# Optimization experiments

Hardware: AMD Instinct MI355X
Metric: run time of the kernel (lower is better)

The kernel has to match this reference:

```python
import jax, jax.numpy as jnp
import numpy as np

GRID_SIZE = 16          # number of spline intervals; G+1 = 17 control points
KH, KW = 3, 3           # kernel size
EPS = 1e-8


def _extract_patches(x, kh, kw):
    """x: (B,H,W,C) -> patches (B,Ho,Wo,C,kh,kw), valid padding, stride 1."""
    B, H, W, C = x.shape
    Ho, Wo = H - kh + 1, W - kw + 1
    rows = []
    for i in range(kh):
        cols = []
        for j in range(kw):
            cols.append(x[:, i:i + Ho, j:j + Wo, :])  # (B,Ho,Wo,C)
        rows.append(jnp.stack(cols, axis=-1))          # (B,Ho,Wo,C,kw)
    return jnp.stack(rows, axis=-2)                    # (B,Ho,Wo,C,kh,kw)


def setup_inputs() -> dict:
    key = jax.random.key(0)
    k1, k2, k3, k4 = jax.random.split(key, 4)
    B, H, W, C, F = 4, 66, 66, 32, 64
    x = jax.random.normal(k1, (B, H, W, C), dtype=jnp.float32)
    control_points = jax.random.normal(k2, (F, C, KH, KW, GRID_SIZE + 1), dtype=jnp.float32) * 0.1
    w_spline = jax.random.normal(k3, (F, C, KH, KW), dtype=jnp.float32) * 0.1
    w_silu = jax.random.normal(k4, (F, C, KH, KW), dtype=jnp.float32) * 0.1
    bias = jnp.zeros((F,), dtype=jnp.float32)
    return {"x": x, "control_points": control_points, "w_spline": w_spline,
            "w_silu": w_silu, "bias": bias}


def reference(x, control_points, w_spline, w_silu, bias):
    # Fixed B-spline grid in [-1, 1]
    grid = jnp.linspace(-1.0, 1.0, GRID_SIZE + 1, dtype=x.dtype)  # (G+1,)
    grid_spacing = 2.0 / GRID_SIZE

    # Patch extraction (valid padding, stride 1)
    patches = _extract_patches(x, KH, KW)  # (B,Ho,Wo,C,kh,kw)

    # Linear B-spline (hat) basis with normalization
    xc = jnp.clip(patches, -1.0, 1.0)
    dist = jnp.abs(xc[..., None] - grid)                     # (B,Ho,Wo,C,kh,kw,G+1)
    w = jnp.maximum(0.0, 1.0 - dist / grid_spacing)
    basis = w / (jnp.sum(w, axis=-1, keepdims=True) + EPS)

    # K(x) = w_spline * spline(x) + w_silu * SiLU(x); reduce over (C,kh,kw) per filter
    cp_eff = w_spline[..., None] * control_points            # (F,C,kh,kw,G+1)
    spline_term = jnp.einsum('bhwcijg,fcijg->bhwf', basis, cp_eff)
    silu_term = jnp.einsum('bhwcij,fcij->bhwf', jax.nn.silu(patches), w_silu)

    return spline_term + silu_term + bias  # (B,Ho,Wo,F)
```

## Files before the change

### kernel.cpp

```cpp
#include <hip/hip_runtime.h>
#include <stdint.h>

typedef _Float16 half8 __attribute__((ext_vector_type(8)));
typedef float f32x16 __attribute__((ext_vector_type(16)));
typedef float f32x4  __attribute__((ext_vector_type(4)));

#define NTH2 340992
#define PREP_BLOCKS (NTH2 / 256)

__global__ __launch_bounds__(256) void kan_prep(
    const float* __restrict__ cp, const float* __restrict__ wspl,
    const float* __restrict__ wsil, _Float16* __restrict__ th2)
{
    int e  = blockIdx.x * 256 + threadIdx.x;
    int p  = e / 18944;
    int r  = e - p * 18944;
    int f  = r / 296;
    int cb = r - f * 296;
    int i  = p / 6;
    int jh = p - i * 6;
    int j  = jh >> 1;
    int h2 = jh & 1;
    float v = 0.0f;
    if (cb < 288) {
        int kk = h2 * 288 + cb;
        int c  = kk / 18;
        int m  = kk - c * 18;
        int base = ((f * 32 + c) * 3 + i) * 3 + j;
        v = (m < 17) ? wspl[base] * cp[base * 17 + m] : wsil[base];
    }
    th2[e] = (_Float16)v;
}

__global__ __launch_bounds__(128) void kan_main(
    const float* __restrict__ x, const _Float16* __restrict__ th2,
    const float* __restrict__ bias, float* __restrict__ out)
{
    __shared__ __align__(16) _Float16 lA[32 * 296];
    __shared__ __align__(16) _Float16 lB[64 * 296];

    const int bx  = blockIdx.x;
    const int ph  = bx >> 8;
    const int row = bx & 255;
    const int b   = row >> 6;
    const int ho  = row & 63;

    const int tid  = threadIdx.x;
    const int wf   = tid >> 6;
    const int lane = tid & 63;
    const int r31  = lane & 31;
    const int kh   = lane >> 5;

    const int ar = tid >> 2;
    const int cq = tid & 3;

    const char* thB = (const char*)th2;
    char* lBc = (char*)lB;
    char* lAc = (char*)lA;

    f32x16 acc;
    {
        float bv = bias[wf * 32 + r31];
#pragma unroll
        for (int r = 0; r < 16; ++r) acc[r] = bv;
    }

    const _Float16* pa = lA + r31 * 296 + kh * 8;
    const _Float16* pb = lB + (wf * 32 + r31) * 296 + kh * 8;

    for (int p = 0; p < 18; ++p) {
        const int i  = p / 6;
        const int jh = p - i * 6;
        const int j  = jh >> 1;
        const int h2 = jh & 1;

        {
            const char* gs = thB + (size_t)p * 37888 + wf * 1024 + lane * 16;
            char* ld = lBc + wf * 1024;
#pragma unroll
            for (int t = 0; t < 18; ++t)
                __builtin_amdgcn_global_load_lds(
                    (const __attribute__((address_space(1))) void*)(gs + t * 2048),
                    (__attribute__((address_space(3))) void*)(ld + t * 2048),
                    16, 0, 0);
            if (wf == 0)
                __builtin_amdgcn_global_load_lds(
                    (const __attribute__((address_space(1))) void*)(gs + 36864),
                    (__attribute__((address_space(3))) void*)(lBc + 36864),
                    16, 0, 0);
        }

        {
            const f32x4 xv = *(const f32x4*)(
                x + ((size_t)((b * 66 + ho + i) * 66 + ph * 32 + ar + j)) * 32
                  + h2 * 16 + cq * 4);
#pragma unroll
            for (int pr = 0; pr < 2; ++pr) {
                union { _Float16 h[36]; uint64_t q[9]; } pk;
#pragma unroll
                for (int d = 0; d < 2; ++d) {
                    float pv = xv[pr * 2 + d];
                    float u  = fmaf(fminf(1.0f, fmaxf(-1.0f, pv)), 8.0f, 8.0f);
#pragma unroll
                    for (int m = 0; m < 17; ++m)
                        pk.h[d * 18 + m] =
                            (_Float16)fmaxf(0.0f, 1.0f - fabsf(u - (float)m));
                    pk.h[d * 18 + 17] = (_Float16)(
                        pv * __builtin_amdgcn_rcpf(1.0f + __expf(-pv)));
                }
                uint64_t* dst = (uint64_t*)(lAc + ar * 592 + cq * 144 + pr * 72);
#pragma unroll
                for (int r = 0; r < 9; ++r) dst[r] = pk.q[r];
            }
        }

        __syncthreads();

#pragma unroll
        for (int s = 0; s < 18; ++s) {
            half8 a  = *(const half8*)(pa + s * 16);
            half8 bf = *(const half8*)(pb + s * 16);
            acc = __builtin_amdgcn_mfma_f32_32x32x16_f16(a, bf, acc, 0, 0, 0);
        }

        __syncthreads();
    }

    float* obase = out
        + ((size_t)((b * 64 + ho) * 64 + ph * 32)) * 64 + wf * 32;
#pragma unroll
    for (int r = 0; r < 16; ++r) {
        int rowD = (r & 3) + 8 * (r >> 2) + 4 * kh;
        obase[(size_t)rowD * 64 + r31] = acc[r];
    }
}

extern "C" void kernel_launch(void* const* d_in, const int* in_sizes, int n_in,
                              void* d_out, int out_size, void* d_ws, size_t ws_size,
                              hipStream_t stream) {
    const float* x    = (const float*)d_in[0];
    const float* cp   = (const float*)d_in[1];
    const float* wspl = (const float*)d_in[2];
    const float* wsil = (const float*)d_in[3];
    const float* bias = (const float*)d_in[4];
    float* out = (float*)d_out;

    _Float16* th2 = (_Float16*)d_ws;

    kan_prep<<<PREP_BLOCKS, 256, 0, stream>>>(cp, wspl, wsil, th2);
    kan_main<<<512, 128, 0, stream>>>(x, th2, bias, out);
}
```

Baseline: 100.5 us.

## Double-buffer weight tiles and split K across waves with smaller stages

The reduction is split into 36 smaller stages instead of 18, and weight tiles are double-buffered in LDS so the next stage's async global-to-LDS load runs while the current stage's MFMAs execute. Each wave now covers all 64 filters but only half of the K slices, and the two partial sums are combined through LDS at the end. The weight layout is reorganised into a padding-free interleaved form to match. The design relies on hand-written waitcnt counts, which is a correctness risk, and it adds more barriers plus a final reduction step.

```diff
diff --git a/kernel.cpp b/kernel.cpp
--- a/kernel.cpp
+++ b/kernel.cpp
@@ -3,32 +3,27 @@
 
 typedef _Float16 half8 __attribute__((ext_vector_type(8)));
 typedef float f32x16 __attribute__((ext_vector_type(16)));
-typedef float f32x4  __attribute__((ext_vector_type(4)));
 
-#define NTH2 340992
-#define PREP_BLOCKS (NTH2 / 256)
+#define NBH (36 * 9216)
+#define PREP_BLOCKS (NBH / 256)
 
 __global__ __launch_bounds__(256) void kan_prep(
     const float* __restrict__ cp, const float* __restrict__ wspl,
     const float* __restrict__ wsil, _Float16* __restrict__ th2)
 {
-    int e  = blockIdx.x * 256 + threadIdx.x;
-    int p  = e / 18944;
-    int r  = e - p * 18944;
-    int f  = r / 296;
-    int cb = r - f * 296;
-    int i  = p / 6;
-    int jh = p - i * 6;
-    int j  = jh >> 1;
-    int h2 = jh & 1;
-    float v = 0.0f;
-    if (cb < 288) {
-        int kk = h2 * 288 + cb;
-        int c  = kk / 18;
-        int m  = kk - c * 18;
-        int base = ((f * 32 + c) * 3 + i) * 3 + j;
-        v = (m < 17) ? wspl[base] * cp[base * 17 + m] : wsil[base];
-    }
+    int e = blockIdx.x * 256 + threadIdx.x;
+    int p = e / 9216;
+    int r = e - p * 9216;
+    int u = r >> 3, h = r & 7;
+    int off = u >> 6, f = u & 63;
+    int i = p / 12;
+    int rr = p - i * 12;
+    int j = rr >> 2, oct = rr & 3;
+    int kk = oct * 144 + off * 8 + h;
+    int c = kk / 18;
+    int m = kk - c * 18;
+    int base = ((f * 32 + c) * 3 + i) * 3 + j;
+    float v = (m < 17) ? wspl[base] * cp[base * 17 + m] : wsil[base];
     th2[e] = (_Float16)v;
 }
 
@@ -36,102 +31,133 @@
     const float* __restrict__ x, const _Float16* __restrict__ th2,
     const float* __restrict__ bias, float* __restrict__ out)
 {
-    __shared__ __align__(16) _Float16 lA[32 * 296];
-    __shared__ __align__(16) _Float16 lB[64 * 296];
+    __shared__ __align__(16) _Float16 lA[32 * 144];
+    __shared__ __align__(16) _Float16 lB[2][64 * 144];
 
-    const int bx  = blockIdx.x;
-    const int ph  = bx >> 8;
-    const int row = bx & 255;
-    const int b   = row >> 6;
-    const int ho  = row & 63;
+    const int bx = blockIdx.x;
+    const int ph = bx & 1;
+    const int row = bx >> 1;
+    const int b = row >> 6;
+    const int ho = row & 63;
 
-    const int tid  = threadIdx.x;
-    const int wf   = tid >> 6;
+    const int tid = threadIdx.x;
+    const int wv = tid >> 6;
     const int lane = tid & 63;
-    const int r31  = lane & 31;
-    const int kh   = lane >> 5;
-
-    const int ar = tid >> 2;
-    const int cq = tid & 3;
+    const int r31 = lane & 31;
+    const int kh = lane >> 5;
+    const int apx = tid >> 2;
+    const int cc = tid & 3;
 
     const char* thB = (const char*)th2;
-    char* lBc = (char*)lB;
-    char* lAc = (char*)lA;
 
-    f32x16 acc;
-    {
-        float bv = bias[wf * 32 + r31];
-#pragma unroll
-        for (int r = 0; r < 16; ++r) acc[r] = bv;
+    const float bv0 = bias[r31];
+    const float bv1 = bias[32 + r31];
+
+#define STAGE(dst, bi)                                                         \
+    {                                                                          \
+        const char* gs_ = thB + (size_t)(bi) * 18432 + lane * 16;              \
+        char* ld_ = (char*)(dst);                                              \
+        _Pragma("unroll")                                                      \
+        for (int t_ = 0; t_ < 9; ++t_) {                                       \
+            int o_ = (t_ * 2 + wv) << 10;                                      \
+            __builtin_amdgcn_global_load_lds(                                  \
+                (const __attribute__((address_space(1))) void*)(gs_ + o_),     \
+                (__attribute__((address_space(3))) void*)(ld_ + o_),           \
+                16, 0, 0);                                                     \
+        }                                                                      \
     }
 
-    const _Float16* pa = lA + r31 * 296 + kh * 8;
-    const _Float16* pb = lB + (wf * 32 + r31) * 296 + kh * 8;
+    auto xaddr = [&](int n) -> const float2* {
+        int i_ = n / 12;
+        int rr_ = n - i_ * 12;
+        int j_ = rr_ >> 2, oct_ = rr_ & 3;
+        return (const float2*)(
+            x + ((size_t)((b * 66 + ho + i_) * 66 + ph * 32 + apx + j_)) * 32
+              + oct_ * 8 + cc * 2);
+    };
 
-    for (int p = 0; p < 18; ++p) {
-        const int i  = p / 6;
-        const int jh = p - i * 6;
-        const int j  = jh >> 1;
-        const int h2 = jh & 1;
+    float2 xc = *xaddr(0);
+    __builtin_amdgcn_sched_barrier(0);
+    STAGE(lB[0], 0)
+    __builtin_amdgcn_sched_barrier(0);
+
+    f32x16 acc0, acc1;
+#pragma unroll
+    for (int r = 0; r < 16; ++r) { acc0[r] = 0.0f; acc1[r] = 0.0f; }
+
+    int cur = 0;
+    for (int p = 0; p < 36; ++p) {
+        float2 xn = xc;
+        if (p < 35) {
+            xn = *xaddr(p + 1);
+            __builtin_amdgcn_sched_barrier(0);
+            STAGE(lB[cur ^ 1], p + 1)
+            __builtin_amdgcn_sched_barrier(0);
+        }
+        {
+            union { _Float16 h[36]; uint64_t q[9]; } pk;
+#pragma unroll
+            for (int d = 0; d < 2; ++d) {
+                float pv = (d == 0) ? xc.x : xc.y;
+                float u = fmaf(fminf(1.0f, fmaxf(-1.0f, pv)), 8.0f, 8.0f);
+#pragma unroll
+                for (int m = 0; m < 17; ++m)
+                    pk.h[d * 18 + m] =
+                        (_Float16)fmaxf(0.0f, 1.0f - fabsf(u - (float)m));
+                pk.h[d * 18 + 17] = (_Float16)(
+                    pv * __builtin_amdgcn_rcpf(1.0f + __expf(-pv)));
+            }
+#pragma unroll
+            for (int t = 0; t < 9; ++t) {
+                int w = 9 * cc + t;
+                *(uint64_t*)((char*)lA + ((w >> 1) << 9) + apx * 16
+                             + ((w & 1) << 3)) = pk.q[t];
+            }
+        }
+        if (p < 35) asm volatile("s_waitcnt vmcnt(10) lgkmcnt(0)" ::: "memory");
+        else        asm volatile("s_waitcnt vmcnt(0) lgkmcnt(0)" ::: "memory");
+        __builtin_amdgcn_s_barrier();
+        __builtin_amdgcn_sched_barrier(0);
 
         {
-            const char* gs = thB + (size_t)p * 37888 + wf * 1024 + lane * 16;
-            char* ld = lBc + wf * 1024;
-#pragma unroll
-            for (int t = 0; t < 18; ++t)
-                __builtin_amdgcn_global_load_lds(
-                    (const __attribute__((address_space(1))) void*)(gs + t * 2048),
-                    (__attribute__((address_space(3))) void*)(ld + t * 2048),
-                    16, 0, 0);
-            if (wf == 0)
-                __builtin_amdgcn_global_load_lds(
-                    (const __attribute__((address_space(1))) void*)(gs + 36864),
-                    (__attribute__((address_space(3))) void*)(lBc + 36864),
-                    16, 0, 0);
-        }
-
-        {
-            const f32x4 xv = *(const f32x4*)(
-                x + ((size_t)((b * 66 + ho + i) * 66 + ph * 32 + ar + j)) * 32
-                  + h2 * 16 + cq * 4);
-#pragma unroll
-            for (int pr = 0; pr < 2; ++pr) {
-                union { _Float16 h[36]; uint64_t q[9]; } pk;
-#pragma unroll
-                for (int d = 0; d < 2; ++d) {
-                    float pv = xv[pr * 2 + d];
-                    float u  = fmaf(fminf(1.0f, fmaxf(-1.0f, pv)), 8.0f, 8.0f);
-#pragma unroll
-                    for (int m = 0; m < 17; ++m)
-                        pk.h[d * 18 + m] =
-                            (_Float16)fmaxf(0.0f, 1.0f - fabsf(u - (float)m));
-                    pk.h[d * 18 + 17] = (_Float16)(
-                        pv * __builtin_amdgcn_rcpf(1.0f + __expf(-pv)));
-                }
-                uint64_t* dst = (uint64_t*)(lAc + ar * 592 + cq * 144 + pr * 72);
-#pragma unroll
-                for (int r = 0; r < 9; ++r) dst[r] = pk.q[r];
+            const char* pbase = (const char*)lB[cur];
+            for (int s = wv; s < 9; s += 2) {
+                const char* pa = (const char*)lA + ((kh + 2 * s) << 9) + r31 * 16;
+                const char* pb = pbase + ((kh + 2 * s) << 10) + r31 * 16;
+                half8 a  = *(const half8*)pa;
+                half8 g0 = *(const half8*)pb;
+                half8 g1 = *(const half8*)(pb + 512);
+                acc0 = __builtin_amdgcn_mfma_f32_32x32x16_f16(a, g0, acc0, 0, 0, 0);
+                acc1 = __builtin_amdgcn_mfma_f32_32x32x16_f16(a, g1, acc1, 0, 0, 0);
             }
         }
+        asm volatile("s_waitcnt lgkmcnt(0)" ::: "memory");
+        __builtin_amdgcn_s_barrier();
+        cur ^= 1;
+        xc = xn;
+    }
+#undef STAGE
 
-        __syncthreads();
-
+    float* red = (float*)lB;
+    if (wv == 1) {
 #pragma unroll
-        for (int s = 0; s < 18; ++s) {
-            half8 a  = *(const half8*)(pa + s * 16);
-            half8 bf = *(const half8*)(pb + s * 16);
-            acc = __builtin_amdgcn_mfma_f32_32x32x16_f16(a, bf, acc, 0, 0, 0);
+        for (int r = 0; r < 16; ++r) {
+            int rowD = (r & 3) + 8 * (r >> 2) + 4 * kh;
+            red[rowD * 64 + r31]      = acc0[r];
+            red[rowD * 64 + 32 + r31] = acc1[r];
         }
-
-        __syncthreads();
     }
-
-    float* obase = out
-        + ((size_t)((b * 64 + ho) * 64 + ph * 32)) * 64 + wf * 32;
+    __syncthreads();
+    if (wv == 0) {
+        float* obase = out + ((size_t)((b * 64 + ho) * 64 + ph * 32)) * 64;
 #pragma unroll
-    for (int r = 0; r < 16; ++r) {
-        int rowD = (r & 3) + 8 * (r >> 2) + 4 * kh;
-        obase[(size_t)rowD * 64 + r31] = acc[r];
+        for (int r = 0; r < 16; ++r) {
+            int rowD = (r & 3) + 8 * (r >> 2) + 4 * kh;
+            obase[(size_t)rowD * 64 + r31] =
+                acc0[r] + red[rowD * 64 + r31] + bv0;
+            obase[(size_t)rowD * 64 + 32 + r31] =
+                acc1[r] + red[rowD * 64 + 32 + r31] + bv1;
+        }
     }
 }
 
```

Result: slower. 105.8 us (+5.3%).
